# Optimization experiments

Hardware: AMD Instinct MI355X
Metric: run time of the kernel (lower is better)

## Reference

```python
import jax, jax.numpy as jnp
import numpy as np

B, S, D = 2, 1024, 1024
NH = 8
QK = D // 2          # qk_dim_factor = 0.5
V = D                # v_dim_factor = 1.0
DQK = QK // NH       # 64
DV = V // NH         # 128
CAP = 15.0
EPS = 1e-6


def soft_cap(t, cap=CAP):
    return cap * jnp.tanh(t / cap)


def setup_inputs() -> dict:
    key = jax.random.key(0)
    ks = jax.random.split(key, 12)
    sc = 0.02
    return {
        "x": jax.random.normal(ks[0], (B, S, D), jnp.float32),
        "Wq": jax.random.normal(ks[1], (QK, D), jnp.float32) * sc,
        "Wk": jax.random.normal(ks[2], (QK, D), jnp.float32) * sc,
        "Wv": jax.random.normal(ks[3], (V, D), jnp.float32) * sc,
        "Wog": jax.random.normal(ks[4], (V, D), jnp.float32) * sc,
        "Wi": jax.random.normal(ks[5], (NH, D), jnp.float32) * sc,
        "bi": jax.random.normal(ks[6], (NH,), jnp.float32) * sc,
        "Wf": jax.random.normal(ks[7], (NH, D), jnp.float32) * sc,
        "bf": jax.random.normal(ks[8], (NH,), jnp.float32) * sc + 3.0,  # forget-gate bias init high
        "ln_w": jnp.ones((NH * DV,), jnp.float32),
        "ln_b": jnp.zeros((NH * DV,), jnp.float32),
        "Wout": jax.random.normal(ks[9], (D, V), jnp.float32) * sc,
    }


def _mlstm_forward(x, Wq, Wk, Wv, Wog, Wi, bi, Wf, bf, ln_w, ln_b, Wout):
    Bx, Sx, _ = x.shape
    # projections
    q = (x @ Wq.T).reshape(Bx, Sx, NH, DQK)
    k = (x @ Wk.T).reshape(Bx, Sx, NH, DQK)
    v = (x @ Wv.T).reshape(Bx, Sx, NH, DV)
    o_preact = x @ Wog.T                                   # [B,S,V]
    i_pre = soft_cap(x @ Wi.T + bi)                        # [B,S,NH]
    f_pre = soft_cap(x @ Wf.T + bf)                        # [B,S,NH]

    # scan over time: move S to leading axis
    qT = jnp.moveaxis(q, 1, 0)   # [S,B,NH,DQK]
    kT = jnp.moveaxis(k, 1, 0)
    vT = jnp.moveaxis(v, 1, 0)   # [S,B,NH,DV]
    iT = jnp.moveaxis(i_pre, 1, 0)  # [S,B,NH]
    fT = jnp.moveaxis(f_pre, 1, 0)

    qk_scale = DQK ** -0.5

    def step(carry, inp):
        C, n, m = carry                       # C:[B,NH,DQK,DV] n:[B,NH,DQK] m:[B,NH]
        q_t, k_t, v_t, i_t, f_t = inp
        m_new = jnp.maximum(f_t + m, i_t)
        f_act = jnp.exp(f_t + m - m_new)      # [B,NH]
        i_act = jnp.exp(i_t - m_new)
        C = f_act[..., None, None] * C + i_act[..., None, None] * (k_t[..., :, None] * v_t[..., None, :])
        n = f_act[..., None] * n + i_act[..., None] * k_t
        qs = q_t * qk_scale
        num = jnp.einsum('bhk,bhkv->bhv', qs, C)
        qn = jnp.einsum('bhk,bhk->bh', qs, n)
        denom = jnp.maximum(jnp.abs(qn), jnp.exp(-m_new)) + 1e-6
        h_t = num / denom[..., None]          # [B,NH,DV]
        return (C, n, m_new), h_t

    C0 = jnp.zeros((Bx, NH, DQK, DV), x.dtype)
    n0 = jnp.zeros((Bx, NH, DQK), x.dtype)
    m0 = jnp.zeros((Bx, NH), x.dtype)
    _, hs = jax.lax.scan(step, (C0, n0, m0), (qT, kT, vT, iT, fT))
    h = jnp.moveaxis(hs, 0, 1).reshape(Bx, Sx, NH * DV)    # [B,S,V]

    # multi-head layer norm over flattened (NH*DV) dim
    mu = jnp.mean(h, axis=-1, keepdims=True)
    var = jnp.mean((h - mu) ** 2, axis=-1, keepdims=True)
    h_norm = (h - mu) * jax.lax.rsqrt(var + EPS) * ln_w + ln_b

    h_out = jax.nn.sigmoid(o_preact) * h_norm
    y = h_out @ Wout.T
    return y


def reference(x, Wq, Wk, Wv, Wog, Wi, bi, Wf, bf, ln_w, ln_b, Wout):
    return _mlstm_forward(x, Wq, Wk, Wv, Wog, Wi, bi, Wf, bf, ln_w, ln_b, Wout)
```

## Files before the change

kernel.cpp:

```cpp
#include <hip/hip_runtime.h>
#include <math.h>

#define SEQ  1024
#define DM   1024
#define NHD  8
#define DQKD 64
#define DVD  128
#define QKD  512
#define VD   1024
#define NB   2
#define VOC  2048

typedef __attribute__((ext_vector_type(8))) short bf16x8;
typedef __attribute__((ext_vector_type(4))) float f32x4;

__device__ __forceinline__ float softcap(float t) {
    return 15.0f * tanhf(t * (1.0f / 15.0f));
}

__device__ __forceinline__ unsigned short f2bf(float f) {
    union { float f; unsigned u; } v; v.f = f;
    unsigned r = v.u + 0x7FFFu + ((v.u >> 16) & 1u);
    return (unsigned short)(r >> 16);
}

__global__ __launch_bounds__(256) void cvt4_kernel(
    const float* __restrict__ s0, unsigned short* __restrict__ d0,
    const float* __restrict__ s1, unsigned short* __restrict__ d1,
    const float* __restrict__ s2, unsigned short* __restrict__ d2,
    const float* __restrict__ s3, unsigned short* __restrict__ d3) {
    int bx = blockIdx.x;
    const float* s; unsigned short* d; int i;
    if (bx < 2048)      { s = s0; d = d0; i = bx * 256 + threadIdx.x; }
    else if (bx < 3072) { s = s1; d = d1; i = (bx - 2048) * 256 + threadIdx.x; }
    else if (bx < 4096) { s = s2; d = d2; i = (bx - 3072) * 256 + threadIdx.x; }
    else                { s = s3; d = d3; i = (bx - 4096) * 256 + threadIdx.x; }
    float4 v = ((const float4*)s)[i];
    ushort4 o;
    o.x = f2bf(v.x); o.y = f2bf(v.y); o.z = f2bf(v.z); o.w = f2bf(v.w);
    ((ushort4*)d)[i] = o;
}

__global__ __launch_bounds__(256) void gates_kernel(
    const float* __restrict__ x,
    const float* __restrict__ Wi, const float* __restrict__ bi,
    const float* __restrict__ Wf, const float* __restrict__ bf,
    float* __restrict__ ipre, float* __restrict__ fpre) {
    int wid = threadIdx.x >> 6, lane = threadIdx.x & 63;
    int row = blockIdx.x * 4 + wid;
    int b = row >> 10, t = row & 1023;
    const float* xr = x + (size_t)row * DM;
    float ai[NHD] = {}, af[NHD] = {};
    for (int d = lane; d < DM; d += 64) {
        float xv = xr[d];
#pragma unroll
        for (int h = 0; h < NHD; ++h) {
            ai[h] = fmaf(xv, Wi[h * DM + d], ai[h]);
            af[h] = fmaf(xv, Wf[h * DM + d], af[h]);
        }
    }
#pragma unroll
    for (int h = 0; h < NHD; ++h) {
        for (int off = 32; off > 0; off >>= 1) {
            ai[h] += __shfl_xor(ai[h], off);
            af[h] += __shfl_xor(af[h], off);
        }
    }
    if (lane == 0) {
#pragma unroll
        for (int h = 0; h < NHD; ++h) {
            ipre[((b * NHD + h) << 10) + t] = softcap(ai[h] + bi[h]);
            fpre[((b * NHD + h) << 10) + t] = softcap(af[h] + bf[h]);
        }
    }
}

__global__ __launch_bounds__(1024) void scan_kernel(
    const float* __restrict__ ipre, const float* __restrict__ fpre,
    float* __restrict__ gv, float* __restrict__ Mrow,
    float* __restrict__ sufg, float* __restrict__ expnegm) {
    __shared__ float ws1[16], ws2[16], ws3[16];
    int t = threadIdx.x, bh = blockIdx.x;
    int base = bh << 10;
    int lane = t & 63, wid = t >> 6;
    float s = fpre[base + t];
#pragma unroll
    for (int off = 1; off < 64; off <<= 1) {
        float o = __shfl_up(s, off);
        if (lane >= off) s += o;
    }
    if (lane == 63) ws1[wid] = s;
    __syncthreads();
    float bsum = 0.0f;
#pragma unroll
    for (int w = 0; w < 16; ++w) { float v = ws1[w]; if (w < wid) bsum += v; }
    float cumF = s + bsum;
    float g = ipre[base + t] - cumF;
    gv[base + t] = g;
    float m = g;
#pragma unroll
    for (int off = 1; off < 64; off <<= 1) {
        float o = __shfl_up(m, off);
        if (lane >= off) m = fmaxf(m, o);
    }
    if (lane == 63) ws2[wid] = m;
    __syncthreads();
    float bmax = -1e30f;
#pragma unroll
    for (int w = 0; w < 16; ++w) { float v = ws2[w]; if (w < wid) bmax = fmaxf(bmax, v); }
    float Mt = fmaxf(0.0f, fmaxf(m, bmax));
    Mrow[base + t] = Mt;
    expnegm[base + t] = expf(-(cumF + Mt));
    float sm = g;
#pragma unroll
    for (int off = 1; off < 64; off <<= 1) {
        float o = __shfl_down(sm, off);
        if (lane + off < 64) sm = fmaxf(sm, o);
    }
    if (lane == 0) ws3[wid] = sm;
    __syncthreads();
    float amax = -1e30f;
#pragma unroll
    for (int w = 0; w < 16; ++w) { float v = ws3[w]; if (w > wid) amax = fmaxf(amax, v); }
    sufg[base + t] = fmaxf(sm, amax);
}

#define QBM 64
#define QBN 64
#define QBK 16
__global__ __launch_bounds__(512) void qk_gemm_kernel(
    const float* __restrict__ x,
    const float* __restrict__ Wq, const float* __restrict__ Wk,
    float* __restrict__ qb, float* __restrict__ kb) {
    __shared__ __align__(16) float As[QBK][QBM + 4];
    __shared__ __align__(16) float Bs[QBK][QBN + 4];
    int bx = blockIdx.x;
    const float* W; float* C; int col0;
    if (bx < 8) { W = Wq; C = qb; col0 = bx * QBN; }
    else        { W = Wk; C = kb; col0 = (bx - 8) * QBN; }
    int tid = threadIdx.x;
    int row0 = blockIdx.y * QBM;
    int tx = tid & 15, ty = tid >> 4;
    int sr = (tid & 255) >> 2, sc = tid & 3;
    bool stageA = tid < 256;
    const float* P = stageA ? x + (size_t)(row0 + sr) * DM + sc * 4
                            : W + (size_t)(col0 + sr) * DM + sc * 4;
    float acc[2][4] = {};
    for (int k0 = 0; k0 < DM; k0 += QBK) {
        float4 v4 = *(const float4*)(P + k0);
        if (stageA) {
            As[sc * 4 + 0][sr] = v4.x; As[sc * 4 + 1][sr] = v4.y;
            As[sc * 4 + 2][sr] = v4.z; As[sc * 4 + 3][sr] = v4.w;
        } else {
            Bs[sc * 4 + 0][sr] = v4.x; Bs[sc * 4 + 1][sr] = v4.y;
            Bs[sc * 4 + 2][sr] = v4.z; Bs[sc * 4 + 3][sr] = v4.w;
        }
        __syncthreads();
#pragma unroll
        for (int kk = 0; kk < QBK; ++kk) {
            float a0 = As[kk][ty * 2 + 0];
            float a1 = As[kk][ty * 2 + 1];
            float4 bv = *(const float4*)(&Bs[kk][tx * 4]);
            float br[4] = {bv.x, bv.y, bv.z, bv.w};
#pragma unroll
            for (int j = 0; j < 4; ++j) {
                acc[0][j] = fmaf(a0, br[j], acc[0][j]);
                acc[1][j] = fmaf(a1, br[j], acc[1][j]);
            }
        }
        __syncthreads();
    }
#pragma unroll
    for (int i = 0; i < 2; ++i) {
        float4 o4 = {acc[i][0], acc[i][1], acc[i][2], acc[i][3]};
        *(float4*)(C + (size_t)(row0 + ty * 2 + i) * QKD + col0 + tx * 4) = o4;
    }
}

__global__ __launch_bounds__(256) void mfma_nt_kernel(
    const unsigned short* __restrict__ A, const unsigned short* __restrict__ B,
    float* __restrict__ C, int ldc, int K) {
    __shared__ __align__(16) unsigned short As[128 * 32];
    __shared__ __align__(16) unsigned short Bs[128 * 32];
    int tid = threadIdx.x;
    int w = tid >> 6, l = tid & 63;
    int wr = w >> 1, wc = w & 1;
    int r0 = blockIdx.y * 128, c0 = blockIdx.x * 128;
    f32x4 acc[4][4] = {};
    for (int k0 = 0; k0 < K; k0 += 32) {
#pragma unroll
        for (int it = 0; it < 2; ++it) {
            const unsigned short* ga = A + (size_t)(r0 + it * 64 + w * 16 + (l >> 2)) * K + k0 + ((l & 3) << 3);
            __builtin_amdgcn_global_load_lds(
                (const __attribute__((address_space(1))) unsigned int*)ga,
                (__attribute__((address_space(3))) unsigned int*)&As[(it * 64 + w * 16) * 32],
                16, 0, 0);
            const unsigned short* gb = B + (size_t)(c0 + it * 64 + w * 16 + (l >> 2)) * K + k0 + ((l & 3) << 3);
            __builtin_amdgcn_global_load_lds(
                (const __attribute__((address_space(1))) unsigned int*)gb,
                (__attribute__((address_space(3))) unsigned int*)&Bs[(it * 64 + w * 16) * 32],
                16, 0, 0);
        }
        __syncthreads();
        bf16x8 af[4], bfr[4];
#pragma unroll
        for (int mi = 0; mi < 4; ++mi)
            af[mi] = *(const bf16x8*)&As[(wr * 64 + mi * 16 + (l & 15)) * 32 + ((l >> 4) << 3)];
#pragma unroll
        for (int ni = 0; ni < 4; ++ni)
            bfr[ni] = *(const bf16x8*)&Bs[(wc * 64 + ni * 16 + (l & 15)) * 32 + ((l >> 4) << 3)];
#pragma unroll
        for (int mi = 0; mi < 4; ++mi)
#pragma unroll
            for (int ni = 0; ni < 4; ++ni)
                acc[mi][ni] = __builtin_amdgcn_mfma_f32_16x16x32_bf16(af[mi], bfr[ni], acc[mi][ni], 0, 0, 0);
        __syncthreads();
    }
#pragma unroll
    for (int mi = 0; mi < 4; ++mi) {
#pragma unroll
        for (int ni = 0; ni < 4; ++ni) {
            int row = r0 + wr * 64 + mi * 16 + ((l >> 4) << 2);
            int col = c0 + wc * 64 + ni * 16 + (l & 15);
            float* cp = C + (size_t)row * ldc + col;
#pragma unroll
            for (int j = 0; j < 4; ++j) cp[(size_t)j * ldc] = acc[mi][ni][j];
        }
    }
}

__global__ __launch_bounds__(256) void attn_kernel(
    const float* __restrict__ q, const float* __restrict__ k,
    const float* __restrict__ vob, const float* __restrict__ gv,
    const float* __restrict__ Mrow, const float* __restrict__ sufg,
    const float* __restrict__ expnegm, float* __restrict__ hbuf) {
    int wid = threadIdx.x >> 6, lane = threadIdx.x & 63;
    int bh = blockIdx.x;
    int t = blockIdx.y * 4 + wid;
    int b = bh >> 3, h = bh & 7;
    int base = bh << 10;
    float Mt = Mrow[base + t];
    float qs = q[(size_t)(b * SEQ + t) * QKD + h * DQKD + lane] * 0.125f;
    float num0 = 0.0f, num1 = 0.0f, qn = 0.0f;
    for (int j = 0; j <= t; ++j) {
        if ((j & 15) == 0) {
            if (sufg[base + j] - Mt < -60.0f) break;
        }
        float kj = k[(size_t)(b * SEQ + j) * QKD + h * DQKD + lane];
        float s = qs * kj;
#pragma unroll
        for (int off = 32; off > 0; off >>= 1) s += __shfl_xor(s, off);
        float w = expf(gv[base + j] - Mt);
        float p = w * s;
        qn += p;
        const float* vr = vob + (size_t)(b * SEQ + j) * VOC + h * DVD;
        num0 = fmaf(p, vr[lane], num0);
        num1 = fmaf(p, vr[lane + 64], num1);
    }
    float denom = fmaxf(fabsf(qn), expnegm[base + t]) + 1e-6f;
    float* hr = hbuf + (size_t)(b * SEQ + t) * VD + h * DVD;
    hr[lane] = num0 / denom;
    hr[lane + 64] = num1 / denom;
}

__global__ __launch_bounds__(256) void ln_gate_kernel(
    const float* __restrict__ hbuf, const float* __restrict__ vob,
    const float* __restrict__ lnw, const float* __restrict__ lnb,
    unsigned short* __restrict__ hgbf) {
    int row = blockIdx.x, tid = threadIdx.x;
    float4 hv = ((const float4*)(hbuf + (size_t)row * VD))[tid];
    float s1 = hv.x + hv.y + hv.z + hv.w;
    float s2 = hv.x * hv.x + hv.y * hv.y + hv.z * hv.z + hv.w * hv.w;
    for (int off = 32; off > 0; off >>= 1) {
        s1 += __shfl_xor(s1, off);
        s2 += __shfl_xor(s2, off);
    }
    __shared__ float w1[4], w2[4];
    int wid = tid >> 6, lane = tid & 63;
    if (lane == 0) { w1[wid] = s1; w2[wid] = s2; }
    __syncthreads();
    s1 = w1[0] + w1[1] + w1[2] + w1[3];
    s2 = w2[0] + w2[1] + w2[2] + w2[3];
    float mean = s1 * (1.0f / 1024.0f);
    float var = s2 * (1.0f / 1024.0f) - mean * mean;
    float rs = rsqrtf(var + 1e-6f);
    float4 ov = ((const float4*)(vob + (size_t)row * VOC + VD))[tid];
    float4 wv = ((const float4*)lnw)[tid];
    float4 bv = ((const float4*)lnb)[tid];
    float ox = (1.0f / (1.0f + expf(-ov.x))) * ((hv.x - mean) * rs * wv.x + bv.x);
    float oy = (1.0f / (1.0f + expf(-ov.y))) * ((hv.y - mean) * rs * wv.y + bv.y);
    float oz = (1.0f / (1.0f + expf(-ov.z))) * ((hv.z - mean) * rs * wv.z + bv.z);
    float ow = (1.0f / (1.0f + expf(-ov.w))) * ((hv.w - mean) * rs * wv.w + bv.w);
    ushort4 o4;
    o4.x = f2bf(ox); o4.y = f2bf(oy); o4.z = f2bf(oz); o4.w = f2bf(ow);
    ((ushort4*)(hgbf + (size_t)row * VD))[tid] = o4;
}

extern "C" void kernel_launch(void* const* d_in, const int* in_sizes, int n_in,
                              void* d_out, int out_size, void* d_ws, size_t ws_size,
                              hipStream_t stream) {
    const float* x    = (const float*)d_in[0];
    const float* Wq   = (const float*)d_in[1];
    const float* Wk   = (const float*)d_in[2];
    const float* Wv   = (const float*)d_in[3];
    const float* Wog  = (const float*)d_in[4];
    const float* Wi   = (const float*)d_in[5];
    const float* bi   = (const float*)d_in[6];
    const float* Wf   = (const float*)d_in[7];
    const float* bf   = (const float*)d_in[8];
    const float* lnw  = (const float*)d_in[9];
    const float* lnb  = (const float*)d_in[10];
    const float* Wout = (const float*)d_in[11];
    float* out = (float*)d_out;

    float* ws = (float*)d_ws;
    const size_t BH   = (size_t)NB * NHD * SEQ;
    const size_t ROWS = (size_t)NB * SEQ;
    float* ipre = ws;
    float* fpre = ipre + BH;
    float* gv   = fpre + BH;
    float* Mrow = gv + BH;
    float* sufg = Mrow + BH;
    float* enm  = sufg + BH;
    float* qb   = enm + BH;
    float* kb   = qb + ROWS * QKD;
    float* vob  = kb + ROWS * QKD;
    unsigned short* xbf   = (unsigned short*)(vob + ROWS * VOC);
    unsigned short* Wvobf = xbf + ROWS * DM;
    unsigned short* Wobf  = Wvobf + (size_t)VOC * DM;
    unsigned short* hgbf  = Wobf + (size_t)DM * VD;
    float* hb = out;

    cvt4_kernel<<<5120, 256, 0, stream>>>(x, xbf,
                                          Wv, Wvobf,
                                          Wog, Wvobf + (size_t)VD * DM,
                                          Wout, Wobf);
    gates_kernel<<<512, 256, 0, stream>>>(x, Wi, bi, Wf, bf, ipre, fpre);
    scan_kernel<<<16, 1024, 0, stream>>>(ipre, fpre, gv, Mrow, sufg, enm);
    mfma_nt_kernel<<<dim3(VOC / 128, ROWS / 128), 256, 0, stream>>>(xbf, Wvobf, vob, VOC, DM);
    qk_gemm_kernel<<<dim3(16, ROWS / QBM), 512, 0, stream>>>(x, Wq, Wk, qb, kb);
    attn_kernel<<<dim3(16, SEQ / 4), 256, 0, stream>>>(qb, kb, vob, gv, Mrow, sufg, enm, hb);
    ln_gate_kernel<<<ROWS, 256, 0, stream>>>(hb, vob, lnw, lnb, hgbf);
    mfma_nt_kernel<<<dim3(DM / 128, ROWS / 128), 256, 0, stream>>>(hgbf, Wobf, out, DM, VD);
}
```

Before: 293.9 us.

## Compute Q/K projection with split-bf16 MFMA GEMMs instead of FP32 SIMT GEMM

Replaces the FP32 SIMT Q/K projection kernel with three bf16 MFMA GEMM passes (hi*hi, lo*hi, hi*lo) that emulate near-FP32 precision. Q and K are fused into one output buffer. The conversion kernel now also splits x, Wq and Wk into hi/lo bf16 parts. This trades extra conversion traffic and three launches with read-modify-write accumulation for matrix-core throughput on a GEMM that previously ran on vector FMAs.

```diff
diff --git a/kernel.cpp b/kernel.cpp
--- a/kernel.cpp
+++ b/kernel.cpp
@@ -10,6 +10,7 @@
 #define VD   1024
 #define NB   2
 #define VOC  2048
+#define QKC  1024
 
 typedef __attribute__((ext_vector_type(8))) short bf16x8;
 typedef __attribute__((ext_vector_type(4))) float f32x4;
@@ -23,22 +24,52 @@
     unsigned r = v.u + 0x7FFFu + ((v.u >> 16) & 1u);
     return (unsigned short)(r >> 16);
 }
-
-__global__ __launch_bounds__(256) void cvt4_kernel(
-    const float* __restrict__ s0, unsigned short* __restrict__ d0,
-    const float* __restrict__ s1, unsigned short* __restrict__ d1,
-    const float* __restrict__ s2, unsigned short* __restrict__ d2,
-    const float* __restrict__ s3, unsigned short* __restrict__ d3) {
+__device__ __forceinline__ float bf2f(unsigned short h) {
+    union { unsigned u; float f; } v; v.u = ((unsigned)h) << 16;
+    return v.f;
+}
+
+__global__ __launch_bounds__(256) void cvt_all_kernel(
+    const float* __restrict__ x,  unsigned short* __restrict__ xhi, unsigned short* __restrict__ xlo,
+    const float* __restrict__ Wq, const float* __restrict__ Wk,
+    unsigned short* __restrict__ Wqkhi, unsigned short* __restrict__ Wqklo,
+    const float* __restrict__ Wv,  const float* __restrict__ Wog,
+    unsigned short* __restrict__ Wvobf,
+    const float* __restrict__ Wout, unsigned short* __restrict__ Wobf) {
     int bx = blockIdx.x;
-    const float* s; unsigned short* d; int i;
-    if (bx < 2048)      { s = s0; d = d0; i = bx * 256 + threadIdx.x; }
-    else if (bx < 3072) { s = s1; d = d1; i = (bx - 2048) * 256 + threadIdx.x; }
-    else if (bx < 4096) { s = s2; d = d2; i = (bx - 3072) * 256 + threadIdx.x; }
-    else                { s = s3; d = d3; i = (bx - 4096) * 256 + threadIdx.x; }
-    float4 v = ((const float4*)s)[i];
-    ushort4 o;
-    o.x = f2bf(v.x); o.y = f2bf(v.y); o.z = f2bf(v.z); o.w = f2bf(v.w);
-    ((ushort4*)d)[i] = o;
+    if (bx < 2048) {
+        int i = bx * 256 + threadIdx.x;
+        float4 v = ((const float4*)x)[i];
+        ushort4 hi, lo;
+        hi.x = f2bf(v.x); lo.x = f2bf(v.x - bf2f(hi.x));
+        hi.y = f2bf(v.y); lo.y = f2bf(v.y - bf2f(hi.y));
+        hi.z = f2bf(v.z); lo.z = f2bf(v.z - bf2f(hi.z));
+        hi.w = f2bf(v.w); lo.w = f2bf(v.w - bf2f(hi.w));
+        ((ushort4*)xhi)[i] = hi;
+        ((ushort4*)xlo)[i] = lo;
+    } else if (bx < 3072) {
+        int sb = bx - 2048;
+        const float* src = (sb < 512) ? Wq : Wk;
+        int i = ((sb < 512) ? sb : sb - 512) * 256 + threadIdx.x;
+        int o = sb * 256 + threadIdx.x;
+        float4 v = ((const float4*)src)[i];
+        ushort4 hi, lo;
+        hi.x = f2bf(v.x); lo.x = f2bf(v.x - bf2f(hi.x));
+        hi.y = f2bf(v.y); lo.y = f2bf(v.y - bf2f(hi.y));
+        hi.z = f2bf(v.z); lo.z = f2bf(v.z - bf2f(hi.z));
+        hi.w = f2bf(v.w); lo.w = f2bf(v.w - bf2f(hi.w));
+        ((ushort4*)Wqkhi)[o] = hi;
+        ((ushort4*)Wqklo)[o] = lo;
+    } else {
+        const float* s; unsigned short* d; int i;
+        if (bx < 4096)      { s = Wv;   d = Wvobf;                      i = (bx - 3072) * 256 + threadIdx.x; }
+        else if (bx < 5120) { s = Wog;  d = Wvobf + (size_t)VD * DM;    i = (bx - 4096) * 256 + threadIdx.x; }
+        else                { s = Wout; d = Wobf;                       i = (bx - 5120) * 256 + threadIdx.x; }
+        float4 v = ((const float4*)s)[i];
+        ushort4 o;
+        o.x = f2bf(v.x); o.y = f2bf(v.y); o.z = f2bf(v.z); o.w = f2bf(v.w);
+        ((ushort4*)d)[i] = o;
+    }
 }
 
 __global__ __launch_bounds__(256) void gates_kernel(
@@ -125,61 +156,9 @@
     sufg[base + t] = fmaxf(sm, amax);
 }
 
-#define QBM 64
-#define QBN 64
-#define QBK 16
-__global__ __launch_bounds__(512) void qk_gemm_kernel(
-    const float* __restrict__ x,
-    const float* __restrict__ Wq, const float* __restrict__ Wk,
-    float* __restrict__ qb, float* __restrict__ kb) {
-    __shared__ __align__(16) float As[QBK][QBM + 4];
-    __shared__ __align__(16) float Bs[QBK][QBN + 4];
-    int bx = blockIdx.x;
-    const float* W; float* C; int col0;
-    if (bx < 8) { W = Wq; C = qb; col0 = bx * QBN; }
-    else        { W = Wk; C = kb; col0 = (bx - 8) * QBN; }
-    int tid = threadIdx.x;
-    int row0 = blockIdx.y * QBM;
-    int tx = tid & 15, ty = tid >> 4;
-    int sr = (tid & 255) >> 2, sc = tid & 3;
-    bool stageA = tid < 256;
-    const float* P = stageA ? x + (size_t)(row0 + sr) * DM + sc * 4
-                            : W + (size_t)(col0 + sr) * DM + sc * 4;
-    float acc[2][4] = {};
-    for (int k0 = 0; k0 < DM; k0 += QBK) {
-        float4 v4 = *(const float4*)(P + k0);
-        if (stageA) {
-            As[sc * 4 + 0][sr] = v4.x; As[sc * 4 + 1][sr] = v4.y;
-            As[sc * 4 + 2][sr] = v4.z; As[sc * 4 + 3][sr] = v4.w;
-        } else {
-            Bs[sc * 4 + 0][sr] = v4.x; Bs[sc * 4 + 1][sr] = v4.y;
-            Bs[sc * 4 + 2][sr] = v4.z; Bs[sc * 4 + 3][sr] = v4.w;
-        }
-        __syncthreads();
-#pragma unroll
-        for (int kk = 0; kk < QBK; ++kk) {
-            float a0 = As[kk][ty * 2 + 0];
-            float a1 = As[kk][ty * 2 + 1];
-            float4 bv = *(const float4*)(&Bs[kk][tx * 4]);
-            float br[4] = {bv.x, bv.y, bv.z, bv.w};
-#pragma unroll
-            for (int j = 0; j < 4; ++j) {
-                acc[0][j] = fmaf(a0, br[j], acc[0][j]);
-                acc[1][j] = fmaf(a1, br[j], acc[1][j]);
-            }
-        }
-        __syncthreads();
-    }
-#pragma unroll
-    for (int i = 0; i < 2; ++i) {
-        float4 o4 = {acc[i][0], acc[i][1], acc[i][2], acc[i][3]};
-        *(float4*)(C + (size_t)(row0 + ty * 2 + i) * QKD + col0 + tx * 4) = o4;
-    }
-}
-
 __global__ __launch_bounds__(256) void mfma_nt_kernel(
     const unsigned short* __restrict__ A, const unsigned short* __restrict__ B,
-    float* __restrict__ C, int ldc, int K) {
+    float* __restrict__ C, int ldc, int K, int accFlag) {
     __shared__ __align__(16) unsigned short As[128 * 32];
     __shared__ __align__(16) unsigned short Bs[128 * 32];
     int tid = threadIdx.x;
@@ -223,30 +202,35 @@
             int row = r0 + wr * 64 + mi * 16 + ((l >> 4) << 2);
             int col = c0 + wc * 64 + ni * 16 + (l & 15);
             float* cp = C + (size_t)row * ldc + col;
-#pragma unroll
-            for (int j = 0; j < 4; ++j) cp[(size_t)j * ldc] = acc[mi][ni][j];
+            if (accFlag) {
+#pragma unroll
+                for (int j = 0; j < 4; ++j) cp[(size_t)j * ldc] += acc[mi][ni][j];
+            } else {
+#pragma unroll
+                for (int j = 0; j < 4; ++j) cp[(size_t)j * ldc] = acc[mi][ni][j];
+            }
         }
     }
 }
 
 __global__ __launch_bounds__(256) void attn_kernel(
-    const float* __restrict__ q, const float* __restrict__ k,
-    const float* __restrict__ vob, const float* __restrict__ gv,
-    const float* __restrict__ Mrow, const float* __restrict__ sufg,
-    const float* __restrict__ expnegm, float* __restrict__ hbuf) {
+    const float* __restrict__ qkb, const float* __restrict__ vob,
+    const float* __restrict__ gv, const float* __restrict__ Mrow,
+    const float* __restrict__ sufg, const float* __restrict__ expnegm,
+    float* __restrict__ hbuf) {
     int wid = threadIdx.x >> 6, lane = threadIdx.x & 63;
     int bh = blockIdx.x;
     int t = blockIdx.y * 4 + wid;
     int b = bh >> 3, h = bh & 7;
     int base = bh << 10;
     float Mt = Mrow[base + t];
-    float qs = q[(size_t)(b * SEQ + t) * QKD + h * DQKD + lane] * 0.125f;
+    float qs = qkb[(size_t)(b * SEQ + t) * QKC + h * DQKD + lane] * 0.125f;
     float num0 = 0.0f, num1 = 0.0f, qn = 0.0f;
     for (int j = 0; j <= t; ++j) {
         if ((j & 15) == 0) {
             if (sufg[base + j] - Mt < -60.0f) break;
         }
-        float kj = k[(size_t)(b * SEQ + j) * QKD + h * DQKD + lane];
+        float kj = qkb[(size_t)(b * SEQ + j) * QKC + QKD + h * DQKD + lane];
         float s = qs * kj;
 #pragma unroll
         for (int off = 32; off > 0; off >>= 1) s += __shfl_xor(s, off);
@@ -322,24 +306,26 @@
     float* Mrow = gv + BH;
     float* sufg = Mrow + BH;
     float* enm  = sufg + BH;
-    float* qb   = enm + BH;
-    float* kb   = qb + ROWS * QKD;
-    float* vob  = kb + ROWS * QKD;
+    float* qkb  = enm + BH;
+    float* vob  = qkb + ROWS * QKC;
     unsigned short* xbf   = (unsigned short*)(vob + ROWS * VOC);
-    unsigned short* Wvobf = xbf + ROWS * DM;
-    unsigned short* Wobf  = Wvobf + (size_t)VOC * DM;
-    unsigned short* hgbf  = Wobf + (size_t)DM * VD;
+    unsigned short* xlobf = xbf + ROWS * DM;
+    unsigned short* Wvobf = xlobf + ROWS * DM;
+    unsigned short* Wqkhi = Wvobf + (size_t)VOC * DM;
+    unsigned short* Wqklo = Wqkhi + (size_t)QKC * DM;
+    unsigned short* Wobf  = Wqklo + (size_t)QKC * DM;
+    unsigned short* hgbf  = xlobf;
     float* hb = out;
 
-    cvt4_kernel<<<5120, 256, 0, stream>>>(x, xbf,
-                                          Wv, Wvobf,
-                                          Wog, Wvobf + (size_t)VD * DM,
-                                          Wout, Wobf);
+    cvt_all_kernel<<<6144, 256, 0, stream>>>(x, xbf, xlobf, Wq, Wk, Wqkhi, Wqklo,
+                                             Wv, Wog, Wvobf, Wout, Wobf);
     gates_kernel<<<512, 256, 0, stream>>>(x, Wi, bi, Wf, bf, ipre, fpre);
     scan_kernel<<<16, 1024, 0, stream>>>(ipre, fpre, gv, Mrow, sufg, enm);
-    mfma_nt_kernel<<<dim3(VOC / 128, ROWS / 128), 256, 0, stream>>>(xbf, Wvobf, vob, VOC, DM);
-    qk_gemm_kernel<<<dim3(16, ROWS / QBM), 512, 0, stream>>>(x, Wq, Wk, qb, kb);
-    attn_kernel<<<dim3(16, SEQ / 4), 256, 0, stream>>>(qb, kb, vob, gv, Mrow, sufg, enm, hb);
+    mfma_nt_kernel<<<dim3(VOC / 128, ROWS / 128), 256, 0, stream>>>(xbf, Wvobf, vob, VOC, DM, 0);
+    mfma_nt_kernel<<<dim3(QKC / 128, ROWS / 128), 256, 0, stream>>>(xbf,   Wqkhi, qkb, QKC, DM, 0);
+    mfma_nt_kernel<<<dim3(QKC / 128, ROWS / 128), 256, 0, stream>>>(xlobf, Wqkhi, qkb, QKC, DM, 1);
+    mfma_nt_kernel<<<dim3(QKC / 128, ROWS / 128), 256, 0, stream>>>(xbf,   Wqklo, qkb, QKC, DM, 1);
+    attn_kernel<<<dim3(16, SEQ / 4), 256, 0, stream>>>(qkb, vob, gv, Mrow, sufg, enm, hb);
     ln_gate_kernel<<<ROWS, 256, 0, stream>>>(hb, vob, lnw, lnb, hgbf);
-    mfma_nt_kernel<<<dim3(DM / 128, ROWS / 128), 256, 0, stream>>>(hgbf, Wobf, out, DM, VD);
-}
+    mfma_nt_kernel<<<dim3(DM / 128, ROWS / 128), 256, 0, stream>>>(hgbf, Wobf, out, DM, VD, 0);
+}
```

After: 306.6 us. +4.3%, slower.
